# Optimization experiments

Hardware: AMD Instinct MI355X
Metric: run time of the kernel (lower is better)

Reference implementation:

```python
import jax, jax.numpy as jnp
import numpy as np

ATOM_VOC = 128
APO = 128
NHEAD = 16
D_MODEL = 512
BOND_VOC = 32
CHIRAL_VOC = 4
B, L = 4, 384


def setup_inputs() -> dict:
    key = jax.random.key(0)
    ks = jax.random.split(key, 12)
    atoms = jax.random.randint(ks[0], (B, L), 0, ATOM_VOC)
    chirals = jax.random.randint(ks[1], (B, L), 0, CHIRAL_VOC)
    coordinates = jax.random.normal(ks[2], (B, L, 3), dtype=jnp.float32)
    bonds = jax.random.randint(ks[3], (B, L, L), 0, BOND_VOC)
    # embedding tables; padding_idx rows (0) zeroed to match torch padding_idx
    atype_emb = jax.random.normal(ks[4], (ATOM_VOC, D_MODEL), dtype=jnp.float32) * 0.02
    atype_emb = atype_emb.at[0].set(0.0)
    chiral_emb = jax.random.normal(ks[5], (CHIRAL_VOC, D_MODEL), dtype=jnp.float32) * 0.02
    chiral_emb = chiral_emb.at[0].set(0.0)
    apair_w_emb = jax.random.normal(ks[6], (ATOM_VOC * ATOM_VOC, APO), dtype=jnp.float32) * 0.02
    apair_b_emb = jax.random.normal(ks[7], (ATOM_VOC * ATOM_VOC, APO), dtype=jnp.float32) * 0.02
    means = jax.random.normal(ks[8], (APO,), dtype=jnp.float32) * 0.1
    stds = jnp.ones((APO,), dtype=jnp.float32) + jax.random.normal(ks[9], (APO,), dtype=jnp.float32) * 0.1
    bond_emb = jax.random.normal(ks[10], (BOND_VOC, NHEAD), dtype=jnp.float32) * 0.02
    bond_emb = bond_emb.at[0].set(0.0)
    lin_w = jax.random.normal(ks[11], (NHEAD, APO), dtype=jnp.float32) * (1.0 / np.sqrt(APO))
    lin_b = jnp.zeros((NHEAD,), dtype=jnp.float32)
    return dict(atoms=atoms, chirals=chirals, coordinates=coordinates, bonds=bonds,
                atype_emb=atype_emb, chiral_emb=chiral_emb,
                apair_w_emb=apair_w_emb, apair_b_emb=apair_b_emb,
                means=means, stds=stds, bond_emb=bond_emb, lin_w=lin_w, lin_b=lin_b)


def reference(atoms, chirals, coordinates, bonds, atype_emb, chiral_emb,
              apair_w_emb, apair_b_emb, means, stds, bond_emb, lin_w, lin_b):
    # atoms: [b,l] int; coordinates: [b,l,3]; bonds: [b,l,l] int
    atoms_emb = atype_emb[atoms] + chiral_emb[chirals]          # [b,l,d]
    atoms_emb = jnp.transpose(atoms_emb, (1, 0, 2))             # [l,b,d]
    diff = coordinates[:, None, :, :] - coordinates[:, :, None, :]  # [b,l,l,3]
    d2 = jnp.sum(diff * diff, axis=-1)
    distances = jnp.sqrt(d2 + 1e-12)                            # [b,l,l] (eps avoids nan grad on diag)
    apair_idx = atoms[:, None, :] * ATOM_VOC + atoms[:, :, None]  # [b,l,l]
    ap = apair_w_emb[apair_idx] * distances[..., None] + apair_b_emb[apair_idx]  # [b,l,l,apo]
    s = jnp.abs(stds) + 1e-5
    ap = jnp.exp(-0.5 * jnp.square((ap - means) / s)) / (np.sqrt(2 * np.pi) * s)
    ap = jnp.einsum('bijk,hk->bijh', ap, lin_w) + lin_b + bond_emb[bonds]  # [b,l,l,nhead]
    pad = (atoms == 0)[:, None, :, None]                        # mask key atoms (dim 2)
    ap = jnp.where(pad, -jnp.inf, ap)
    ap = jnp.transpose(ap, (0, 3, 1, 2))                        # [b,nhead,l,l]
    return atoms_emb, ap
```

## Files before the change

### kernel.cpp

```cpp
#include <hip/hip_runtime.h>
#include <math.h>
#include <string.h>

#define ATOM_VOC 128
#define APO      128
#define NHEAD    16
#define D_MODEL  512
#define NB       4
#define NL       384

typedef __attribute__((ext_vector_type(8))) short    bf16x8;
typedef __attribute__((ext_vector_type(4))) float    f32x4;
typedef __attribute__((ext_vector_type(4))) unsigned u32x4;

#if __has_builtin(__builtin_amdgcn_exp2f)
#define EXP2F(x) __builtin_amdgcn_exp2f(x)
#else
#define EXP2F(x) exp2f(x)
#endif

#define PACK_DWORDS (ATOM_VOC * ATOM_VOC * APO)
#define BFT_SHORTS  (4 * 4 * 16 * 8)

static __device__ inline unsigned f2bf(float x) {
    unsigned u = __float_as_uint(x);
    u += 0x7fffu + ((u >> 16) & 1u);
    return u >> 16;
}

__global__ __launch_bounds__(128) void pack_kernel(
    const float* __restrict__ apw, const float* __restrict__ apb,
    const float* __restrict__ means, const float* __restrict__ stds,
    const float* __restrict__ lin_w,
    unsigned* __restrict__ pack, unsigned short* __restrict__ bft, int write_bft)
{
    const int k  = threadIdx.x;
    const int v  = blockIdx.x;
    const int ai = blockIdx.y;
    const float s  = fabsf(stds[k]) + 1e-5f;
    const float ag = 0.84932180028802f / s;
    const size_t src = ((size_t)v * ATOM_VOC + ai) * APO + k;
    const float w  = apw[src] * ag;
    const float bb = (apb[src] - means[k]) * ag;
    pack[((size_t)ai * ATOM_VOC + v) * APO + k] = (f2bf(bb) << 16) | f2bf(w);

    if (write_bft && v == 0 && ai == 0) {
#pragma unroll
        for (int half = 0; half < 2; ++half) {
            const int cid  = k + half * 128;
            const int ks   = cid >> 6;
            const int quad = (cid >> 4) & 3;
            const int h    = cid & 15;
            const int kb   = ks * 32 + quad * 8;
            unsigned short tmp[8];
#pragma unroll
            for (int u = 0; u < 8; ++u) {
                const int kk = kb + u;
                float z = 0.3989422804014327f / (fabsf(stds[kk]) + 1e-5f);
                tmp[u] = (unsigned short)f2bf(lin_w[h * APO + kk] * z);
            }
            memcpy(&bft[(size_t)cid * 8], tmp, 16);
        }
    }
}

__global__ __launch_bounds__(256) void atoms_emb_kernel(
    const int* __restrict__ atoms, const int* __restrict__ chirals,
    const float* __restrict__ atype_emb, const float* __restrict__ chiral_emb,
    float* __restrict__ out)
{
    const int D4 = D_MODEL / 4;
    int t = blockIdx.x * 256 + threadIdx.x;
    if (t >= NL * NB * D4) return;
    int d4 = t % D4;
    int bl = t / D4;
    int b  = bl % NB;
    int l  = bl / NB;
    int a  = atoms[b * NL + l];
    int c  = chirals[b * NL + l];
    float4 va = ((const float4*)(atype_emb  + (size_t)a * D_MODEL))[d4];
    float4 vc = ((const float4*)(chiral_emb + (size_t)c * D_MODEL))[d4];
    float4 o;
    o.x = va.x + vc.x; o.y = va.y + vc.y; o.z = va.z + vc.z; o.w = va.w + vc.w;
    ((float4*)out)[t] = o;
}

template <bool USE_BFT>
__global__ __launch_bounds__(512, 4) void ap_kernel(
    const int*            __restrict__ atoms,
    const float*          __restrict__ coords,
    const int*            __restrict__ bonds,
    const unsigned*       __restrict__ pack,
    const unsigned short* __restrict__ bft,
    const float*          __restrict__ stds,
    const float*          __restrict__ bond_emb,
    const float*          __restrict__ lin_w,
    const float*          __restrict__ lin_b,
    float*                __restrict__ out)
{
    const int i    = blockIdx.x;
    const int b    = blockIdx.y;
    const int t    = threadIdx.x;
    const int lane = t & 63;
    const int wave = t >> 6;
    const int h    = lane & 15;
    const int quad = lane >> 4;

    __shared__ unsigned tbl[ATOM_VOC * APO];

    const int ai = atoms[b * NL + i];

    const unsigned* src = pack + (size_t)ai * (ATOM_VOC * APO);
#pragma unroll
    for (int it = 0; it < 8; ++it) {
        int c   = it * 512 + t;
        int v   = c >> 5;
        int c16 = c & 31;
        u32x4 d = ((const u32x4*)src)[c];
        *(u32x4*)&tbl[v * APO + 4 * (c16 ^ (v & 31))] = d;
    }

    bf16x8 bfrag[4];
    if (USE_BFT) {
#pragma unroll
        for (int ks = 0; ks < 4; ++ks)
            memcpy(&bfrag[ks], bft + ((size_t)((ks * 4 + quad) * 16 + h)) * 8, 16);
    } else {
#pragma unroll
        for (int ks = 0; ks < 4; ++ks) {
            unsigned short tmp[8];
#pragma unroll
            for (int u = 0; u < 8; ++u) {
                int k   = ks * 32 + quad * 8 + u;
                float z = 0.3989422804014327f / (fabsf(stds[k]) + 1e-5f);
                tmp[u]  = (unsigned short)f2bf(lin_w[h * APO + k] * z);
            }
            memcpy(&bfrag[ks], tmp, 16);
        }
    }
    const float lbh = lin_b[h];

    const float cix = coords[((size_t)b * NL + i) * 3 + 0];
    const float ciy = coords[((size_t)b * NL + i) * 3 + 1];
    const float ciz = coords[((size_t)b * NL + i) * 3 + 2];

    int   jv[3];
    float jdist[3];
#pragma unroll
    for (int it = 0; it < 3; ++it) {
        const int j = it * 128 + wave * 16 + h;
        jv[it] = atoms[b * NL + j];
        const float dx = coords[((size_t)b * NL + j) * 3 + 0] - cix;
        const float dy = coords[((size_t)b * NL + j) * 3 + 1] - ciy;
        const float dz = coords[((size_t)b * NL + j) * 3 + 2] - ciz;
        jdist[it] = sqrtf(fmaf(dx, dx, fmaf(dy, dy, dz * dz)) + 1e-12f);
    }

    __syncthreads();

    const size_t bondrow = ((size_t)b * NL + i) * NL;
    float* op = out + (((size_t)(b * NHEAD + h)) * NL + i) * NL;

#pragma unroll
    for (int it = 0; it < 3; ++it) {
        const int jt    = it * 128 + wave * 16;
        const int v     = jv[it];
        const float dist = jdist[it];
        const int vx    = v & 31;
        const int vbase = v * APO;

        const int jb = jt + quad * 4;
        int bidx[4], aje[4];
#pragma unroll
        for (int r = 0; r < 4; ++r) {
            bidx[r] = bonds[bondrow + jb + r];
            aje[r]  = atoms[b * NL + jb + r];
        }

        u32x4 pa[8];
#pragma unroll
        for (int cc = 0; cc < 8; ++cc) {
            const int ks    = cc >> 1, e = cc & 1;
            const int chunk = ks * 8 + quad * 2 + e;
            pa[cc] = *(const u32x4*)&tbl[vbase + 4 * (chunk ^ vx)];
        }

        f32x4 acc = {0.f, 0.f, 0.f, 0.f};
#pragma unroll
        for (int ks = 0; ks < 4; ++ks) {
            unsigned pk[8] = {pa[2*ks].x, pa[2*ks].y, pa[2*ks].z, pa[2*ks].w,
                              pa[2*ks+1].x, pa[2*ks+1].y, pa[2*ks+1].z, pa[2*ks+1].w};
            unsigned gg[8];
#pragma unroll
            for (int u = 0; u < 8; ++u) {
                unsigned d = pk[u];
                float wf = __uint_as_float(d << 16);
                float bf = __uint_as_float(d & 0xffff0000u);
                float uu = fmaf(wf, dist, bf);
                float g  = EXP2F(-(uu * uu));
                gg[u] = __float_as_uint(g);
            }
            unsigned afw[4];
#pragma unroll
            for (int p = 0; p < 4; ++p)
                afw[p] = __builtin_amdgcn_perm(gg[2 * p + 1], gg[2 * p], 0x07060302u);
            bf16x8 af;
            memcpy(&af, afw, 16);
            acc = __builtin_amdgcn_mfma_f32_16x16x32_bf16(af, bfrag[ks], acc, 0, 0, 0);
        }

#pragma unroll
        for (int r = 0; r < 4; ++r) {
            float vv = acc[r] + lbh + bond_emb[bidx[r] * NHEAD + h];
            if (aje[r] == 0) vv = -1.0e30f;
            op[jb + r] = vv;
        }
    }
}

extern "C" void kernel_launch(void* const* d_in, const int* in_sizes, int n_in,
                              void* d_out, int out_size, void* d_ws, size_t ws_size,
                              hipStream_t stream)
{
    const int*   atoms      = (const int*)d_in[0];
    const int*   chirals    = (const int*)d_in[1];
    const float* coords     = (const float*)d_in[2];
    const int*   bonds      = (const int*)d_in[3];
    const float* atype_emb  = (const float*)d_in[4];
    const float* chiral_emb = (const float*)d_in[5];
    const float* apw        = (const float*)d_in[6];
    const float* apb        = (const float*)d_in[7];
    const float* means      = (const float*)d_in[8];
    const float* stds       = (const float*)d_in[9];
    const float* bond_emb   = (const float*)d_in[10];
    const float* lin_w      = (const float*)d_in[11];
    const float* lin_b      = (const float*)d_in[12];
    float* out = (float*)d_out;

    unsigned* pack = (unsigned*)d_ws;
    const size_t need = (size_t)PACK_DWORDS * 4 + BFT_SHORTS * 2;
    const bool use_bft = (ws_size >= need);
    unsigned short* bftp = use_bft
        ? (unsigned short*)((char*)d_ws + (size_t)PACK_DWORDS * 4) : nullptr;

    pack_kernel<<<dim3(ATOM_VOC, ATOM_VOC), dim3(APO), 0, stream>>>(
        apw, apb, means, stds, lin_w, pack, bftp, use_bft ? 1 : 0);

    {
        const int total = NL * NB * (D_MODEL / 4);
        atoms_emb_kernel<<<dim3((total + 255) / 256), dim3(256), 0, stream>>>(
            atoms, chirals, atype_emb, chiral_emb, out);
    }
    {
        float* out2 = out + (size_t)NL * NB * D_MODEL;
        if (use_bft)
            ap_kernel<true><<<dim3(NL, NB), dim3(512), 0, stream>>>(
                atoms, coords, bonds, pack, bftp, stds, bond_emb, lin_w, lin_b, out2);
        else
            ap_kernel<false><<<dim3(NL, NB), dim3(512), 0, stream>>>(
                atoms, coords, bonds, pack, bftp, stds, bond_emb, lin_w, lin_b, out2);
    }
}
```

Before: 131.6 us.

## Switch Gaussian basis to packed fp16 math with f16 MFMA and prefetch

Stores the pair weight/bias table as fp16 split into separate w and b halves, so the Gaussian evaluation runs as packed half2 fma/mul/exp2 instead of per-element fp32 with bf16 repacking. The matmul moves to the f16 MFMA, and LDS reads plus bond/atom loads for the next j-tile are software-prefetched into a double buffer. The workspace-size fallback path is removed. This cuts VALU and transcendental work in the hot loop, at the cost of fp16 range and precision in the exponent argument and extra registers for the prefetch buffers.

```diff
diff --git a/kernel.cpp b/kernel.cpp
--- a/kernel.cpp
+++ b/kernel.cpp
@@ -1,4 +1,5 @@
 #include <hip/hip_runtime.h>
+#include <hip/hip_fp16.h>
 #include <math.h>
 #include <string.h>
 
@@ -9,23 +10,16 @@
 #define NB       4
 #define NL       384
 
-typedef __attribute__((ext_vector_type(8))) short    bf16x8;
+typedef __attribute__((ext_vector_type(8))) _Float16 f16x8;
 typedef __attribute__((ext_vector_type(4))) float    f32x4;
 typedef __attribute__((ext_vector_type(4))) unsigned u32x4;
 
-#if __has_builtin(__builtin_amdgcn_exp2f)
-#define EXP2F(x) __builtin_amdgcn_exp2f(x)
-#else
-#define EXP2F(x) exp2f(x)
-#endif
-
 #define PACK_DWORDS (ATOM_VOC * ATOM_VOC * APO)
 #define BFT_SHORTS  (4 * 4 * 16 * 8)
 
-static __device__ inline unsigned f2bf(float x) {
-    unsigned u = __float_as_uint(x);
-    u += 0x7fffu + ((u >> 16) & 1u);
-    return u >> 16;
+static __device__ inline unsigned short f2h(float x) {
+    __half h = __float2half(x);
+    unsigned short u; memcpy(&u, &h, 2); return u;
 }
 
 __global__ __launch_bounds__(128) void pack_kernel(
@@ -34,20 +28,34 @@
     const float* __restrict__ lin_w,
     unsigned* __restrict__ pack, unsigned short* __restrict__ bft, int write_bft)
 {
-    const int k  = threadIdx.x;
-    const int v  = blockIdx.x;
-    const int ai = blockIdx.y;
-    const float s  = fabsf(stds[k]) + 1e-5f;
-    const float ag = 0.84932180028802f / s;
-    const size_t src = ((size_t)v * ATOM_VOC + ai) * APO + k;
-    const float w  = apw[src] * ag;
-    const float bb = (apb[src] - means[k]) * ag;
-    pack[((size_t)ai * ATOM_VOC + v) * APO + k] = (f2bf(bb) << 16) | f2bf(w);
+    const int t    = threadIdx.x;
+    const int v    = blockIdx.x;
+    const int ai   = blockIdx.y;
+    const int half = t >> 6;
+    const int p    = t & 63;
+    const int k0   = 2 * p, k1 = 2 * p + 1;
+
+    const float s0  = fabsf(stds[k0]) + 1e-5f;
+    const float s1  = fabsf(stds[k1]) + 1e-5f;
+    const float ag0 = 0.84932180028802f / s0;
+    const float ag1 = 0.84932180028802f / s1;
+
+    const size_t srcrow = ((size_t)v * ATOM_VOC + ai) * APO;
+    float x0, x1;
+    if (half == 0) {
+        x0 = apw[srcrow + k0] * ag0;
+        x1 = apw[srcrow + k1] * ag1;
+    } else {
+        x0 = (apb[srcrow + k0] - means[k0]) * ag0;
+        x1 = (apb[srcrow + k1] - means[k1]) * ag1;
+    }
+    pack[((size_t)ai * ATOM_VOC + v) * APO + half * 64 + p] =
+        ((unsigned)f2h(x1) << 16) | f2h(x0);
 
     if (write_bft && v == 0 && ai == 0) {
 #pragma unroll
-        for (int half = 0; half < 2; ++half) {
-            const int cid  = k + half * 128;
+        for (int hh = 0; hh < 2; ++hh) {
+            const int cid  = t + hh * 128;
             const int ks   = cid >> 6;
             const int quad = (cid >> 4) & 3;
             const int h    = cid & 15;
@@ -57,7 +65,7 @@
             for (int u = 0; u < 8; ++u) {
                 const int kk = kb + u;
                 float z = 0.3989422804014327f / (fabsf(stds[kk]) + 1e-5f);
-                tmp[u] = (unsigned short)f2bf(lin_w[h * APO + kk] * z);
+                tmp[u] = f2h(lin_w[h * APO + kk] * z);
             }
             memcpy(&bft[(size_t)cid * 8], tmp, 16);
         }
@@ -85,16 +93,13 @@
     ((float4*)out)[t] = o;
 }
 
-template <bool USE_BFT>
 __global__ __launch_bounds__(512, 4) void ap_kernel(
     const int*            __restrict__ atoms,
     const float*          __restrict__ coords,
     const int*            __restrict__ bonds,
     const unsigned*       __restrict__ pack,
     const unsigned short* __restrict__ bft,
-    const float*          __restrict__ stds,
     const float*          __restrict__ bond_emb,
-    const float*          __restrict__ lin_w,
     const float*          __restrict__ lin_b,
     float*                __restrict__ out)
 {
@@ -113,39 +118,27 @@
     const unsigned* src = pack + (size_t)ai * (ATOM_VOC * APO);
 #pragma unroll
     for (int it = 0; it < 8; ++it) {
-        int c   = it * 512 + t;
-        int v   = c >> 5;
-        int c16 = c & 31;
-        u32x4 d = ((const u32x4*)src)[c];
-        *(u32x4*)&tbl[v * APO + 4 * (c16 ^ (v & 31))] = d;
-    }
-
-    bf16x8 bfrag[4];
-    if (USE_BFT) {
-#pragma unroll
-        for (int ks = 0; ks < 4; ++ks)
-            memcpy(&bfrag[ks], bft + ((size_t)((ks * 4 + quad) * 16 + h)) * 8, 16);
-    } else {
-#pragma unroll
-        for (int ks = 0; ks < 4; ++ks) {
-            unsigned short tmp[8];
-#pragma unroll
-            for (int u = 0; u < 8; ++u) {
-                int k   = ks * 32 + quad * 8 + u;
-                float z = 0.3989422804014327f / (fabsf(stds[k]) + 1e-5f);
-                tmp[u]  = (unsigned short)f2bf(lin_w[h * APO + k] * z);
-            }
-            memcpy(&bfrag[ks], tmp, 16);
-        }
-    }
+        int c    = it * 512 + t;
+        int v    = c >> 5;
+        int cc   = c & 31;
+        int hlf  = cc >> 4;
+        int cp   = cc & 15;
+        u32x4 d  = ((const u32x4*)src)[c];
+        *(u32x4*)&tbl[v * APO + hlf * 64 + 4 * (cp ^ (v & 15))] = d;
+    }
+
+    f16x8 bfrag[4];
+#pragma unroll
+    for (int ks = 0; ks < 4; ++ks)
+        memcpy(&bfrag[ks], bft + ((size_t)((ks * 4 + quad) * 16 + h)) * 8, 16);
     const float lbh = lin_b[h];
 
     const float cix = coords[((size_t)b * NL + i) * 3 + 0];
     const float ciy = coords[((size_t)b * NL + i) * 3 + 1];
     const float ciz = coords[((size_t)b * NL + i) * 3 + 2];
 
-    int   jv[3];
-    float jdist[3];
+    int     jv[3];
+    __half2 jd2[3];
 #pragma unroll
     for (int it = 0; it < 3; ++it) {
         const int j = it * 128 + wave * 16 + h;
@@ -153,7 +146,8 @@
         const float dx = coords[((size_t)b * NL + j) * 3 + 0] - cix;
         const float dy = coords[((size_t)b * NL + j) * 3 + 1] - ciy;
         const float dz = coords[((size_t)b * NL + j) * 3 + 2] - ciz;
-        jdist[it] = sqrtf(fmaf(dx, dx, fmaf(dy, dy, dz * dz)) + 1e-12f);
+        jd2[it] = __half2half2(__float2half(
+            sqrtf(fmaf(dx, dx, fmaf(dy, dy, dz * dz)) + 1e-12f)));
     }
 
     __syncthreads();
@@ -161,61 +155,66 @@
     const size_t bondrow = ((size_t)b * NL + i) * NL;
     float* op = out + (((size_t)(b * NHEAD + h)) * NL + i) * NL;
 
+    u32x4 pa[2][8];
+    int   bidx[2][4], aje[2][4];
+
+#define ISSUE(itc, s)                                                         \
+    {                                                                         \
+        const int v_    = jv[itc];                                            \
+        const int vb_   = v_ * APO;                                           \
+        const int vx_   = v_ & 15;                                            \
+        _Pragma("unroll")                                                     \
+        for (int cc = 0; cc < 8; ++cc) {                                      \
+            const int ks_ = cc >> 1, e_ = cc & 1;                             \
+            pa[s][cc] = *(const u32x4*)&tbl[vb_ + e_ * 64 +                   \
+                                           4 * ((ks_ * 4 + quad) ^ vx_)];     \
+        }                                                                     \
+        const int jb_ = itc * 128 + wave * 16 + quad * 4;                     \
+        _Pragma("unroll")                                                     \
+        for (int r = 0; r < 4; ++r) {                                         \
+            bidx[s][r] = bonds[bondrow + jb_ + r];                            \
+            aje[s][r]  = atoms[b * NL + jb_ + r];                             \
+        }                                                                     \
+    }
+
+    ISSUE(0, 0)
+
 #pragma unroll
     for (int it = 0; it < 3; ++it) {
-        const int jt    = it * 128 + wave * 16;
-        const int v     = jv[it];
-        const float dist = jdist[it];
-        const int vx    = v & 31;
-        const int vbase = v * APO;
-
-        const int jb = jt + quad * 4;
-        int bidx[4], aje[4];
+        const int s = it & 1;
+        if (it < 2) ISSUE(it + 1, (it + 1) & 1)
+
+        const __half2 d2 = jd2[it];
+        f32x4 acc = {0.f, 0.f, 0.f, 0.f};
+#pragma unroll
+        for (int ks = 0; ks < 4; ++ks) {
+            const u32x4 wch = pa[s][ks * 2 + 0];
+            const u32x4 bch = pa[s][ks * 2 + 1];
+            unsigned afw[4];
+#pragma unroll
+            for (int q = 0; q < 4; ++q) {
+                __half2 w2, b2;
+                unsigned wd = wch[q], bd = bch[q];
+                memcpy(&w2, &wd, 4); memcpy(&b2, &bd, 4);
+                __half2 u2  = __hfma2(w2, d2, b2);
+                __half2 nm2 = __hmul2(u2, __hneg2(u2));
+                __half2 g2  = h2exp2(nm2);
+                memcpy(&afw[q], &g2, 4);
+            }
+            f16x8 af;
+            memcpy(&af, afw, 16);
+            acc = __builtin_amdgcn_mfma_f32_16x16x32_f16(af, bfrag[ks], acc, 0, 0, 0);
+        }
+
+        const int jb = it * 128 + wave * 16 + quad * 4;
 #pragma unroll
         for (int r = 0; r < 4; ++r) {
-            bidx[r] = bonds[bondrow + jb + r];
-            aje[r]  = atoms[b * NL + jb + r];
-        }
-
-        u32x4 pa[8];
-#pragma unroll
-        for (int cc = 0; cc < 8; ++cc) {
-            const int ks    = cc >> 1, e = cc & 1;
-            const int chunk = ks * 8 + quad * 2 + e;
-            pa[cc] = *(const u32x4*)&tbl[vbase + 4 * (chunk ^ vx)];
-        }
-
-        f32x4 acc = {0.f, 0.f, 0.f, 0.f};
-#pragma unroll
-        for (int ks = 0; ks < 4; ++ks) {
-            unsigned pk[8] = {pa[2*ks].x, pa[2*ks].y, pa[2*ks].z, pa[2*ks].w,
-                              pa[2*ks+1].x, pa[2*ks+1].y, pa[2*ks+1].z, pa[2*ks+1].w};
-            unsigned gg[8];
-#pragma unroll
-            for (int u = 0; u < 8; ++u) {
-                unsigned d = pk[u];
-                float wf = __uint_as_float(d << 16);
-                float bf = __uint_as_float(d & 0xffff0000u);
-                float uu = fmaf(wf, dist, bf);
-                float g  = EXP2F(-(uu * uu));
-                gg[u] = __float_as_uint(g);
-            }
-            unsigned afw[4];
-#pragma unroll
-            for (int p = 0; p < 4; ++p)
-                afw[p] = __builtin_amdgcn_perm(gg[2 * p + 1], gg[2 * p], 0x07060302u);
-            bf16x8 af;
-            memcpy(&af, afw, 16);
-            acc = __builtin_amdgcn_mfma_f32_16x16x32_bf16(af, bfrag[ks], acc, 0, 0, 0);
-        }
-
-#pragma unroll
-        for (int r = 0; r < 4; ++r) {
-            float vv = acc[r] + lbh + bond_emb[bidx[r] * NHEAD + h];
-            if (aje[r] == 0) vv = -1.0e30f;
+            float vv = acc[r] + lbh + bond_emb[bidx[s][r] * NHEAD + h];
+            if (aje[s][r] == 0) vv = -1.0e30f;
             op[jb + r] = vv;
         }
     }
+#undef ISSUE
 }
 
 extern "C" void kernel_launch(void* const* d_in, const int* in_sizes, int n_in,
@@ -238,13 +237,10 @@
     float* out = (float*)d_out;
 
     unsigned* pack = (unsigned*)d_ws;
-    const size_t need = (size_t)PACK_DWORDS * 4 + BFT_SHORTS * 2;
-    const bool use_bft = (ws_size >= need);
-    unsigned short* bftp = use_bft
-        ? (unsigned short*)((char*)d_ws + (size_t)PACK_DWORDS * 4) : nullptr;
-
-    pack_kernel<<<dim3(ATOM_VOC, ATOM_VOC), dim3(APO), 0, stream>>>(
-        apw, apb, means, stds, lin_w, pack, bftp, use_bft ? 1 : 0);
+    unsigned short* bftp = (unsigned short*)((char*)d_ws + (size_t)PACK_DWORDS * 4);
+
+    pack_kernel<<<dim3(ATOM_VOC, ATOM_VOC), dim3(128), 0, stream>>>(
+        apw, apb, means, stds, lin_w, pack, bftp, 1);
 
     {
         const int total = NL * NB * (D_MODEL / 4);
@@ -253,11 +249,7 @@
     }
     {
         float* out2 = out + (size_t)NL * NB * D_MODEL;
-        if (use_bft)
-            ap_kernel<true><<<dim3(NL, NB), dim3(512), 0, stream>>>(
-                atoms, coords, bonds, pack, bftp, stds, bond_emb, lin_w, lin_b, out2);
-        else
-            ap_kernel<false><<<dim3(NL, NB), dim3(512), 0, stream>>>(
-                atoms, coords, bonds, pack, bftp, stds, bond_emb, lin_w, lin_b, out2);
-    }
-}
+        ap_kernel<<<dim3(NL, NB), dim3(512), 0, stream>>>(
+            atoms, coords, bonds, pack, bftp, bond_emb, lin_b, out2);
+    }
+}
```

Measured after the change: 135.6 us. 1.03x slower.
